# Optimization experiments

Measured on AMD Instinct MI355X. Metric: run time of the kernel, lower is better.

## Reference

```python
import jax, jax.numpy as jnp
import numpy as np
import math

BATCH, D_MODEL, D_STATE, SEQ_L = 8, 256, 64, 2048


def setup_inputs() -> dict:
    key = jax.random.key(0)
    k0, k1, k2, k3 = jax.random.split(key, 4)
    x = jax.random.normal(k0, (BATCH, D_MODEL, SEQ_L), dtype=jnp.float32)
    # A = -exp(A_real) - 1j*A_imag  (S4D-Lin style init: A = -0.5 + i*pi*n)
    A_real = jnp.full((D_MODEL, D_STATE), jnp.log(0.5), dtype=jnp.float32)
    A_imag = -jnp.broadcast_to(math.pi * jnp.arange(D_STATE, dtype=jnp.float32), (D_MODEL, D_STATE))
    # B, C stored as real view of complex: (1, H, N, 2)
    B = jax.random.normal(k1, (1, D_MODEL, D_STATE, 2), dtype=jnp.float32)
    C = jax.random.normal(k2, (1, D_MODEL, D_STATE, 2), dtype=jnp.float32)
    # inv_dt: log-uniform in [log(1e-3), log(1e-1)], shape (H, 1)
    u = jax.random.uniform(k3, (D_MODEL, 1), dtype=jnp.float32)
    inv_dt = u * (math.log(0.1) - math.log(0.001)) + math.log(0.001)
    return {"x": x, "A_real": A_real, "A_imag": A_imag, "B": B, "C": C, "inv_dt": inv_dt}


def reference(x, A_real, A_imag, B, C, inv_dt):
    L = x.shape[-1]
    # --- _get_params ---
    A = -jnp.exp(A_real) - 1j * A_imag            # (H, N) complex poles
    dt = jnp.exp(inv_dt)                           # (H, 1)
    Bc = B[..., 0] + 1j * B[..., 1]                # (1, H, N)
    Cc = C[..., 0] + 1j * C[..., 1]                # (1, H, N)
    # --- compute_kernel ---
    dtA = dt * A                                   # (H, N) = log of discrete-time pole
    Ceff = (Bc * Cc) * (jnp.exp(dtA) - 1.0) / A    # (1, H, N)
    # log-Vandermonde: K = 2*Re sum_n Ceff * exp(dtA)^l  -> (1, H, L)
    ell = jnp.arange(L, dtype=jnp.float32)
    vand = jnp.exp(dtA[:, :, None] * ell)          # (H, N, L) complex
    k = 2.0 * jnp.real(jnp.einsum('chn,hnl->chl', Ceff, vand))  # (1, H, L)
    # --- FFT convolution ---
    n = 2 * L
    k_f = jnp.fft.rfft(k, n=n)                     # (1, H, L+1)
    x_f = jnp.fft.rfft(x, n=n)                     # (B, H, L+1)
    y_f = jnp.einsum('bhl,chl->bchl', x_f, k_f)    # (B, 1, H, L+1)
    y = jnp.fft.irfft(y_f, n=n)[..., :L]           # (B, 1, H, L)
    return jax.nn.relu(y)
```

## Files before the change

kernel.cpp:

```cpp
#include <hip/hip_runtime.h>


#define B_ 8
#define H_ 256
#define N_ 64
#define L_ 2048
#define Q_ 64
#define NC_ 32
#define COLS_ 128
#define PKSTR_ 68
#define PLSTR_ 72

typedef __attribute__((ext_vector_type(8))) short bf16x8;
typedef __attribute__((ext_vector_type(4))) float f32x4;

#define WS_W1R  0
#define WS_W1I  (WS_W1R + 2097152)
#define WS_TL   (WS_W1I + 2097152)
#define WS_W2R  (WS_TL  + 2097152)
#define WS_W2I  (WS_W2R + 2097152)
#define WS_E    (WS_W2I + 2097152)

#if defined(__has_builtin)
#  if __has_builtin(__builtin_amdgcn_cvt_pk_bf16_f32)
#    define HAVE_CVT_PK 1
#  endif
#endif

__device__ __forceinline__ unsigned short bf16_rne(float f) {
    unsigned int u = __float_as_uint(f);
    u += 0x7FFF + ((u >> 16) & 1);
    return (unsigned short)(u >> 16);
}
__device__ __forceinline__ float bf16_to_f(unsigned short h) {
    return __uint_as_float(((unsigned int)h) << 16);
}
__device__ __forceinline__ unsigned int pack_bf16x2(float a, float b) {
#ifdef HAVE_CVT_PK
    typedef __bf16 bf16v2 __attribute__((ext_vector_type(2)));
    bf16v2 p = __builtin_amdgcn_cvt_pk_bf16_f32(a, b);
    return __builtin_bit_cast(unsigned int, p);
#else
    unsigned int ua = __float_as_uint(a);
    ua += 0x7FFF + ((ua >> 16) & 1);
    unsigned int ub = __float_as_uint(b);
    ub += 0x7FFF + ((ub >> 16) & 1);
    return (ua >> 16) | (ub & 0xFFFF0000u);
#endif
}

__global__ __launch_bounds__(256) void s4d_prep(
    const float* __restrict__ A_real, const float* __restrict__ A_imag,
    const float* __restrict__ Bmat, const float* __restrict__ Cmat,
    const float* __restrict__ inv_dt,
    unsigned short* __restrict__ W1sr, unsigned short* __restrict__ W1si,
    unsigned short* __restrict__ TLs,
    unsigned short* __restrict__ W2sr, unsigned short* __restrict__ W2si,
    float2* __restrict__ Earr)
{
    __shared__ float qr_l[65 * 66];
    __shared__ float qi_l[65 * 66];
    __shared__ float klds[64];

    const int h   = blockIdx.x;
    const int tid = threadIdx.x;
    const int n   = tid >> 2;
    const int blk = tid & 3;
    const int hn  = h * N_ + n;

    const float Ar = -expf(A_real[hn]);
    const float Ai = -A_imag[hn];
    const float dtv = expf(inv_dt[h]);
    const float dr = dtv * Ar;
    const float di = dtv * Ai;
    const float ew = expf(dr);
    float sdi, cdi;
    sincosf(di, &sdi, &cdi);
    const float wr = ew * cdi;
    const float wi = ew * sdi;
    const float em1r = wr - 1.0f;
    const float em1i = wi;
    const float invden = 1.0f / (Ar * Ar + Ai * Ai);
    const float tr = (em1r * Ar + em1i * Ai) * invden;
    const float ti = (em1i * Ar - em1r * Ai) * invden;
    const float br = Bmat[2 * hn], bi = Bmat[2 * hn + 1];
    const float cr = Cmat[2 * hn], ci = Cmat[2 * hn + 1];
    const float bcr = br * cr - bi * ci;
    const float bci = br * ci + bi * cr;
    const float Cr = 2.0f * (bcr * tr - bci * ti);
    const float Ci = 2.0f * (bcr * ti + bci * tr);

    {
        const int m0 = 48 - 16 * blk;
        const float e0 = expf((float)m0 * dr);
        float s0, c0;
        sincosf((float)m0 * di, &s0, &c0);
        float pr = e0 * c0, pi = e0 * s0;
        union { unsigned short u16[16]; uint4 q[2]; } tr_, ti_;
        #pragma unroll
        for (int i = 0; i < 16; ++i) {
            tr_.u16[15 - i] = bf16_rne(pr);
            ti_.u16[15 - i] = bf16_rne(pi);
            const float npr = pr * wr - pi * wi;
            pi = pr * wi + pi * wr;
            pr = npr;
        }
        uint4* d0 = (uint4*)(W1sr + (size_t)h * 4096 + n * 64 + blk * 16);
        d0[0] = tr_.q[0]; d0[1] = tr_.q[1];
        uint4* d1 = (uint4*)(W1si + (size_t)h * 4096 + n * 64 + blk * 16);
        d1[0] = ti_.q[0]; d1[1] = ti_.q[1];
    }

    {
        const int m0   = blk * 17;
        const int mcnt = (blk == 3) ? 14 : 17;
        const float e0 = expf((float)m0 * dr);
        float s0, c0;
        sincosf((float)m0 * di, &s0, &c0);
        float pr = e0 * c0, pi = e0 * s0;
        for (int i = 0; i < mcnt; ++i) {
            const int m = m0 + i;
            qr_l[m * 66 + n] = Cr * pr - Ci * pi;
            qi_l[m * 66 + n] = Cr * pi + Ci * pr;
            const float npr = pr * wr - pi * wi;
            pi = pr * wi + pi * wr;
            pr = npr;
        }
    }
    __syncthreads();

    if (tid < 64) {
        float s = 0.0f;
        for (int j = 0; j < 64; ++j) s += qr_l[tid * 66 + j];
        klds[tid] = s;

        const int hn2 = h * N_ + tid;
        const float Ar2 = -expf(A_real[hn2]);
        const float Ai2 = -A_imag[hn2];
        const float e64 = expf(64.0f * dtv * Ar2);
        float s64, c64;
        sincosf(64.0f * dtv * (-Ai2) * -1.0f, &s64, &c64);
        Earr[hn2] = make_float2(e64 * c64, e64 * s64);
    }
    __syncthreads();

    {
        const int t = tid >> 2;
        union { unsigned short u16[16]; uint4 q[2]; } a_, b_;
        #pragma unroll
        for (int i = 0; i < 16; ++i) {
            const int j = blk * 16 + i;
            const int d = t - j;
            a_.u16[i] = bf16_rne(d >= 0 ? klds[d >= 0 ? d : 0] : 0.0f);
        }
        uint4* dtl = (uint4*)(TLs + (size_t)h * 4096 + t * 64 + blk * 16);
        dtl[0] = a_.q[0]; dtl[1] = a_.q[1];

        #pragma unroll
        for (int i = 0; i < 16; ++i) {
            const int nn = blk * 16 + i;
            a_.u16[i] = bf16_rne(qr_l[(t + 1) * 66 + nn]);
            b_.u16[i] = bf16_rne(-qi_l[(t + 1) * 66 + nn]);
        }
        uint4* d2r = (uint4*)(W2sr + (size_t)h * 4096 + t * 64 + blk * 16);
        d2r[0] = a_.q[0]; d2r[1] = a_.q[1];
        uint4* d2i = (uint4*)(W2si + (size_t)h * 4096 + t * 64 + blk * 16);
        d2i[0] = b_.q[0]; d2i[1] = b_.q[1];
    }
}

__global__ __launch_bounds__(256) void s4d_fused(
    const float* __restrict__ x,
    const float2* __restrict__ Earr,
    const unsigned short* __restrict__ W1sr, const unsigned short* __restrict__ W1si,
    const unsigned short* __restrict__ TLs,
    const unsigned short* __restrict__ W2sr, const unsigned short* __restrict__ W2si,
    float* __restrict__ out)
{
    __shared__ char smem[64512];
    unsigned int*   vpk  = (unsigned int*)smem;
    unsigned short* spr  = (unsigned short*)smem;
    unsigned short* spi  = (unsigned short*)(smem + COLS_ * PLSTR_ * 2);
    unsigned short* wreg = (unsigned short*)(smem + COLS_ * PLSTR_ * 4);

    const int h     = blockIdx.x >> 1;
    const int bhalf = blockIdx.x & 1;
    const int tid   = threadIdx.x;
    const int lane  = tid & 63;
    const int wv    = tid >> 6;
    const int colw  = wv * 32;
    const int l15   = lane & 15;
    const int quad  = lane >> 4;

    {
        const unsigned short* s0 = W1sr + (size_t)h * 4096;
        const unsigned short* s1 = W1si + (size_t)h * 4096;
        #pragma unroll
        for (int rep = 0; rep < 2; ++rep) {
            const int idx = rep * 256 + tid;
            const int row = idx >> 3, c8 = (idx & 7) * 8;
            *(uint4*)(wreg + row * PLSTR_ + c8) = *(const uint4*)(s0 + idx * 8);
            *(uint4*)(wreg + 4608 + row * PLSTR_ + c8) = *(const uint4*)(s1 + idx * 8);
        }
    }

    bf16x8 xhi[2][2], xlo[2][2];
    #pragma unroll
    for (int mt = 0; mt < 2; ++mt) {
        const int bc = colw + mt * 16 + l15;
        const int b  = bhalf * 4 + (bc >> 5);
        const int c  = bc & 31;
        const float* xp = x + ((size_t)(b * H_ + h)) * L_ + c * Q_;
        #pragma unroll
        for (int kk = 0; kk < 2; ++kk) {
            const int j0 = kk * 32 + quad * 8;
            const float4 f0 = *(const float4*)(xp + j0);
            const float4 f1 = *(const float4*)(xp + j0 + 4);
            float f[8] = {f0.x, f0.y, f0.z, f0.w, f1.x, f1.y, f1.z, f1.w};
            union { unsigned int u[4]; bf16x8 v; } hi, lo;
            #pragma unroll
            for (int p = 0; p < 4; ++p) {
                const unsigned int hp = pack_bf16x2(f[2 * p], f[2 * p + 1]);
                hi.u[p] = hp;
                const float h0 = __uint_as_float(hp << 16);
                const float h1 = __uint_as_float(hp & 0xFFFF0000u);
                lo.u[p] = pack_bf16x2(f[2 * p] - h0, f[2 * p + 1] - h1);
            }
            xhi[mt][kk] = hi.v;
            xlo[mt][kk] = lo.v;
        }
    }

    const float2 E = Earr[h * N_ + lane];
    const float Er = E.x, Ei = E.y;

    __syncthreads();

    {
        f32x4 accr[2][4], acci[2][4];
        #pragma unroll
        for (int a = 0; a < 2; ++a)
            #pragma unroll
            for (int b = 0; b < 4; ++b) { accr[a][b] = (f32x4)0.0f; acci[a][b] = (f32x4)0.0f; }

        #pragma unroll
        for (int nt = 0; nt < 4; ++nt) {
            const int n = nt * 16 + l15;
            bf16x8 brf[2], bif[2];
            #pragma unroll
            for (int kk = 0; kk < 2; ++kk) {
                const int j0 = kk * 32 + quad * 8;
                brf[kk] = *(const bf16x8*)(wreg + n * PLSTR_ + j0);
                bif[kk] = *(const bf16x8*)(wreg + 4608 + n * PLSTR_ + j0);
            }
            #pragma unroll
            for (int mt = 0; mt < 2; ++mt)
                #pragma unroll
                for (int kk = 0; kk < 2; ++kk) {
                    accr[mt][nt] = __builtin_amdgcn_mfma_f32_16x16x32_bf16(
                        xhi[mt][kk], brf[kk], accr[mt][nt], 0, 0, 0);
                    acci[mt][nt] = __builtin_amdgcn_mfma_f32_16x16x32_bf16(
                        xhi[mt][kk], bif[kk], acci[mt][nt], 0, 0, 0);
                }
        }

        #pragma unroll
        for (int mt = 0; mt < 2; ++mt)
            #pragma unroll
            for (int nt = 0; nt < 4; ++nt)
                #pragma unroll
                for (int r = 0; r < 4; ++r) {
                    const int bc = colw + mt * 16 + quad * 4 + r;
                    const int n  = nt * 16 + l15;
                    vpk[bc * PKSTR_ + n] =
                        pack_bf16x2(accr[mt][nt][r], acci[mt][nt][r]);
                }
    }
    __syncthreads();

    {
        unsigned int vv[NC_];
        const unsigned int* vp = &vpk[(wv * NC_) * PKSTR_ + lane];
        #pragma unroll
        for (int c = 0; c < NC_; ++c) vv[c] = vp[c * PKSTR_];

        {
            const unsigned short* s0 = TLs  + (size_t)h * 4096;
            const unsigned short* s1 = W2sr + (size_t)h * 4096;
            const unsigned short* s2 = W2si + (size_t)h * 4096;
            #pragma unroll
            for (int rep = 0; rep < 2; ++rep) {
                const int idx = rep * 256 + tid;
                const int row = idx >> 3, c8 = (idx & 7) * 8;
                *(uint4*)(wreg + row * PLSTR_ + c8) = *(const uint4*)(s0 + idx * 8);
                *(uint4*)(wreg + 4608 + row * PLSTR_ + c8) = *(const uint4*)(s1 + idx * 8);
                *(uint4*)(wreg + 9216 + row * PLSTR_ + c8) = *(const uint4*)(s2 + idx * 8);
            }
        }
        __syncthreads();

        float sr = 0.0f, si = 0.0f;
        unsigned short* pr = &spr[(wv * NC_) * PLSTR_ + lane];
        unsigned short* pi = &spi[(wv * NC_) * PLSTR_ + lane];
        #pragma unroll
        for (int c = 0; c < NC_; ++c) {
            const float vr = __uint_as_float(vv[c] << 16);
            const float vi = __uint_as_float(vv[c] & 0xFFFF0000u);
            const unsigned int sp2 = pack_bf16x2(sr, si);
            pr[c * PLSTR_] = (unsigned short)(sp2 & 0xFFFFu);
            pi[c * PLSTR_] = (unsigned short)(sp2 >> 16);
            const float nsr = fmaf(Er, sr, fmaf(-Ei, si, vr));
            si = fmaf(Ei, sr, fmaf(Er, si, vi));
            sr = nsr;
        }
    }
    __syncthreads();

    {
        bf16x8 sr8[2][2], si8[2][2];
        #pragma unroll
        for (int mt = 0; mt < 2; ++mt) {
            const int bc = colw + mt * 16 + l15;
            #pragma unroll
            for (int kk = 0; kk < 2; ++kk) {
                const int j0 = kk * 32 + quad * 8;
                sr8[mt][kk] = *(const bf16x8*)(&spr[bc * PLSTR_ + j0]);
                si8[mt][kk] = *(const bf16x8*)(&spi[bc * PLSTR_ + j0]);
            }
        }

        f32x4 acc[2][4];
        #pragma unroll
        for (int a = 0; a < 2; ++a)
            #pragma unroll
            for (int t = 0; t < 4; ++t) acc[a][t] = (f32x4)0.0f;

        #pragma unroll
        for (int tt = 0; tt < 4; ++tt) {
            const int t = tt * 16 + l15;
            bf16x8 btl[2], bwr[2], bwi[2];
            #pragma unroll
            for (int kk = 0; kk < 2; ++kk) {
                const int j0 = kk * 32 + quad * 8;
                btl[kk] = *(const bf16x8*)(wreg + t * PLSTR_ + j0);
                bwr[kk] = *(const bf16x8*)(wreg + 4608 + t * PLSTR_ + j0);
                bwi[kk] = *(const bf16x8*)(wreg + 9216 + t * PLSTR_ + j0);
            }
            #pragma unroll
            for (int mt = 0; mt < 2; ++mt)
                #pragma unroll
                for (int kk = 0; kk < 2; ++kk) {
                    acc[mt][tt] = __builtin_amdgcn_mfma_f32_16x16x32_bf16(
                        xhi[mt][kk], btl[kk], acc[mt][tt], 0, 0, 0);
                    acc[mt][tt] = __builtin_amdgcn_mfma_f32_16x16x32_bf16(
                        xlo[mt][kk], btl[kk], acc[mt][tt], 0, 0, 0);
                    acc[mt][tt] = __builtin_amdgcn_mfma_f32_16x16x32_bf16(
                        sr8[mt][kk], bwr[kk], acc[mt][tt], 0, 0, 0);
                    acc[mt][tt] = __builtin_amdgcn_mfma_f32_16x16x32_bf16(
                        si8[mt][kk], bwi[kk], acc[mt][tt], 0, 0, 0);
                }
        }

        #pragma unroll
        for (int mt = 0; mt < 2; ++mt)
            #pragma unroll
            for (int tt = 0; tt < 4; ++tt)
                #pragma unroll
                for (int r = 0; r < 4; ++r) {
                    const int bc = colw + mt * 16 + quad * 4 + r;
                    const int b  = bhalf * 4 + (bc >> 5);
                    const int c  = bc & 31;
                    const int t  = tt * 16 + l15;
                    out[((size_t)(b * H_ + h)) * L_ + c * Q_ + t] =
                        fmaxf(acc[mt][tt][r], 0.0f);
                }
    }
}

extern "C" void kernel_launch(void* const* d_in, const int* in_sizes, int n_in,
                              void* d_out, int out_size, void* d_ws, size_t ws_size,
                              hipStream_t stream) {
    const float* x      = (const float*)d_in[0];
    const float* A_real = (const float*)d_in[1];
    const float* A_imag = (const float*)d_in[2];
    const float* Bmat   = (const float*)d_in[3];
    const float* Cmat   = (const float*)d_in[4];
    const float* inv_dt = (const float*)d_in[5];
    float* out = (float*)d_out;

    char* ws = (char*)d_ws;
    unsigned short* W1sr = (unsigned short*)(ws + WS_W1R);
    unsigned short* W1si = (unsigned short*)(ws + WS_W1I);
    unsigned short* TLs  = (unsigned short*)(ws + WS_TL);
    unsigned short* W2sr = (unsigned short*)(ws + WS_W2R);
    unsigned short* W2si = (unsigned short*)(ws + WS_W2I);
    float2*         Earr = (float2*)(ws + WS_E);

    s4d_prep<<<dim3(H_), dim3(256), 0, stream>>>(
        A_real, A_imag, Bmat, Cmat, inv_dt, W1sr, W1si, TLs, W2sr, W2si, Earr);
    s4d_fused<<<dim3(H_ * 2), dim3(256), 0, stream>>>(
        x, Earr, W1sr, W1si, TLs, W2sr, W2si, out);
}
```

Measured before the change: 90.21 us.

## Fuse parameter prep kernel into main kernel, building weights directly in LDS

```diff
diff --git a/kernel.cpp b/kernel.cpp
--- a/kernel.cpp
+++ b/kernel.cpp
@@ -14,13 +14,6 @@
 typedef __attribute__((ext_vector_type(8))) short bf16x8;
 typedef __attribute__((ext_vector_type(4))) float f32x4;
 
-#define WS_W1R  0
-#define WS_W1I  (WS_W1R + 2097152)
-#define WS_TL   (WS_W1I + 2097152)
-#define WS_W2R  (WS_TL  + 2097152)
-#define WS_W2I  (WS_W2R + 2097152)
-#define WS_E    (WS_W2I + 2097152)
-
 #if defined(__has_builtin)
 #  if __has_builtin(__builtin_amdgcn_cvt_pk_bf16_f32)
 #    define HAVE_CVT_PK 1
@@ -31,9 +24,6 @@
     unsigned int u = __float_as_uint(f);
     u += 0x7FFF + ((u >> 16) & 1);
     return (unsigned short)(u >> 16);
-}
-__device__ __forceinline__ float bf16_to_f(unsigned short h) {
-    return __uint_as_float(((unsigned int)h) << 16);
 }
 __device__ __forceinline__ unsigned int pack_bf16x2(float a, float b) {
 #ifdef HAVE_CVT_PK
@@ -49,139 +39,24 @@
 #endif
 }
 
-__global__ __launch_bounds__(256) void s4d_prep(
+__global__ __launch_bounds__(256, 2) void s4d_one(
+    const float* __restrict__ x,
     const float* __restrict__ A_real, const float* __restrict__ A_imag,
     const float* __restrict__ Bmat, const float* __restrict__ Cmat,
     const float* __restrict__ inv_dt,
-    unsigned short* __restrict__ W1sr, unsigned short* __restrict__ W1si,
-    unsigned short* __restrict__ TLs,
-    unsigned short* __restrict__ W2sr, unsigned short* __restrict__ W2si,
-    float2* __restrict__ Earr)
-{
-    __shared__ float qr_l[65 * 66];
-    __shared__ float qi_l[65 * 66];
-    __shared__ float klds[64];
-
-    const int h   = blockIdx.x;
-    const int tid = threadIdx.x;
-    const int n   = tid >> 2;
-    const int blk = tid & 3;
-    const int hn  = h * N_ + n;
-
-    const float Ar = -expf(A_real[hn]);
-    const float Ai = -A_imag[hn];
-    const float dtv = expf(inv_dt[h]);
-    const float dr = dtv * Ar;
-    const float di = dtv * Ai;
-    const float ew = expf(dr);
-    float sdi, cdi;
-    sincosf(di, &sdi, &cdi);
-    const float wr = ew * cdi;
-    const float wi = ew * sdi;
-    const float em1r = wr - 1.0f;
-    const float em1i = wi;
-    const float invden = 1.0f / (Ar * Ar + Ai * Ai);
-    const float tr = (em1r * Ar + em1i * Ai) * invden;
-    const float ti = (em1i * Ar - em1r * Ai) * invden;
-    const float br = Bmat[2 * hn], bi = Bmat[2 * hn + 1];
-    const float cr = Cmat[2 * hn], ci = Cmat[2 * hn + 1];
-    const float bcr = br * cr - bi * ci;
-    const float bci = br * ci + bi * cr;
-    const float Cr = 2.0f * (bcr * tr - bci * ti);
-    const float Ci = 2.0f * (bcr * ti + bci * tr);
-
-    {
-        const int m0 = 48 - 16 * blk;
-        const float e0 = expf((float)m0 * dr);
-        float s0, c0;
-        sincosf((float)m0 * di, &s0, &c0);
-        float pr = e0 * c0, pi = e0 * s0;
-        union { unsigned short u16[16]; uint4 q[2]; } tr_, ti_;
-        #pragma unroll
-        for (int i = 0; i < 16; ++i) {
-            tr_.u16[15 - i] = bf16_rne(pr);
-            ti_.u16[15 - i] = bf16_rne(pi);
-            const float npr = pr * wr - pi * wi;
-            pi = pr * wi + pi * wr;
-            pr = npr;
-        }
-        uint4* d0 = (uint4*)(W1sr + (size_t)h * 4096 + n * 64 + blk * 16);
-        d0[0] = tr_.q[0]; d0[1] = tr_.q[1];
-        uint4* d1 = (uint4*)(W1si + (size_t)h * 4096 + n * 64 + blk * 16);
-        d1[0] = ti_.q[0]; d1[1] = ti_.q[1];
-    }
-
-    {
-        const int m0   = blk * 17;
-        const int mcnt = (blk == 3) ? 14 : 17;
-        const float e0 = expf((float)m0 * dr);
-        float s0, c0;
-        sincosf((float)m0 * di, &s0, &c0);
-        float pr = e0 * c0, pi = e0 * s0;
-        for (int i = 0; i < mcnt; ++i) {
-            const int m = m0 + i;
-            qr_l[m * 66 + n] = Cr * pr - Ci * pi;
-            qi_l[m * 66 + n] = Cr * pi + Ci * pr;
-            const float npr = pr * wr - pi * wi;
-            pi = pr * wi + pi * wr;
-            pr = npr;
-        }
-    }
-    __syncthreads();
-
-    if (tid < 64) {
-        float s = 0.0f;
-        for (int j = 0; j < 64; ++j) s += qr_l[tid * 66 + j];
-        klds[tid] = s;
-
-        const int hn2 = h * N_ + tid;
-        const float Ar2 = -expf(A_real[hn2]);
-        const float Ai2 = -A_imag[hn2];
-        const float e64 = expf(64.0f * dtv * Ar2);
-        float s64, c64;
-        sincosf(64.0f * dtv * (-Ai2) * -1.0f, &s64, &c64);
-        Earr[hn2] = make_float2(e64 * c64, e64 * s64);
-    }
-    __syncthreads();
-
-    {
-        const int t = tid >> 2;
-        union { unsigned short u16[16]; uint4 q[2]; } a_, b_;
-        #pragma unroll
-        for (int i = 0; i < 16; ++i) {
-            const int j = blk * 16 + i;
-            const int d = t - j;
-            a_.u16[i] = bf16_rne(d >= 0 ? klds[d >= 0 ? d : 0] : 0.0f);
-        }
-        uint4* dtl = (uint4*)(TLs + (size_t)h * 4096 + t * 64 + blk * 16);
-        dtl[0] = a_.q[0]; dtl[1] = a_.q[1];
-
-        #pragma unroll
-        for (int i = 0; i < 16; ++i) {
-            const int nn = blk * 16 + i;
-            a_.u16[i] = bf16_rne(qr_l[(t + 1) * 66 + nn]);
-            b_.u16[i] = bf16_rne(-qi_l[(t + 1) * 66 + nn]);
-        }
-        uint4* d2r = (uint4*)(W2sr + (size_t)h * 4096 + t * 64 + blk * 16);
-        d2r[0] = a_.q[0]; d2r[1] = a_.q[1];
-        uint4* d2i = (uint4*)(W2si + (size_t)h * 4096 + t * 64 + blk * 16);
-        d2i[0] = b_.q[0]; d2i[1] = b_.q[1];
-    }
-}
-
-__global__ __launch_bounds__(256) void s4d_fused(
-    const float* __restrict__ x,
-    const float2* __restrict__ Earr,
-    const unsigned short* __restrict__ W1sr, const unsigned short* __restrict__ W1si,
-    const unsigned short* __restrict__ TLs,
-    const unsigned short* __restrict__ W2sr, const unsigned short* __restrict__ W2si,
     float* __restrict__ out)
 {
-    __shared__ char smem[64512];
+    __shared__ __align__(16) char smem[81664];
+    float*          qr_l = (float*)smem;
+    float*          qi_l = (float*)(smem + 17160);
     unsigned int*   vpk  = (unsigned int*)smem;
     unsigned short* spr  = (unsigned short*)smem;
-    unsigned short* spi  = (unsigned short*)(smem + COLS_ * PLSTR_ * 2);
-    unsigned short* wreg = (unsigned short*)(smem + COLS_ * PLSTR_ * 4);
+    unsigned short* spi  = (unsigned short*)(smem + 18432);
+    unsigned short* w1r  = (unsigned short*)(smem + 34816);
+    unsigned short* w1i  = (unsigned short*)(smem + 44032);
+    unsigned short* wreg = (unsigned short*)(smem + 53248);
+    float2*         eLDS = (float2*)(smem + 80896);
+    float*          klds = (float*)(smem + 81408);
 
     const int h     = blockIdx.x >> 1;
     const int bhalf = blockIdx.x & 1;
@@ -192,19 +67,7 @@
     const int l15   = lane & 15;
     const int quad  = lane >> 4;
 
-    {
-        const unsigned short* s0 = W1sr + (size_t)h * 4096;
-        const unsigned short* s1 = W1si + (size_t)h * 4096;
-        #pragma unroll
-        for (int rep = 0; rep < 2; ++rep) {
-            const int idx = rep * 256 + tid;
-            const int row = idx >> 3, c8 = (idx & 7) * 8;
-            *(uint4*)(wreg + row * PLSTR_ + c8) = *(const uint4*)(s0 + idx * 8);
-            *(uint4*)(wreg + 4608 + row * PLSTR_ + c8) = *(const uint4*)(s1 + idx * 8);
-        }
-    }
-
-    bf16x8 xhi[2][2], xlo[2][2];
+    float4 xraw[2][2][2];
     #pragma unroll
     for (int mt = 0; mt < 2; ++mt) {
         const int bc = colw + mt * 16 + l15;
@@ -214,8 +77,128 @@
         #pragma unroll
         for (int kk = 0; kk < 2; ++kk) {
             const int j0 = kk * 32 + quad * 8;
-            const float4 f0 = *(const float4*)(xp + j0);
-            const float4 f1 = *(const float4*)(xp + j0 + 4);
+            xraw[mt][kk][0] = *(const float4*)(xp + j0);
+            xraw[mt][kk][1] = *(const float4*)(xp + j0 + 4);
+        }
+    }
+
+    const int n   = tid >> 2;
+    const int blk = tid & 3;
+    const int hn  = h * N_ + n;
+    {
+        const float Ar = -expf(A_real[hn]);
+        const float Ai = -A_imag[hn];
+        const float dtv = expf(inv_dt[h]);
+        const float dr = dtv * Ar;
+        const float di = dtv * Ai;
+        const float ew = expf(dr);
+        float sdi, cdi;
+        sincosf(di, &sdi, &cdi);
+        const float wr = ew * cdi;
+        const float wi = ew * sdi;
+        const float em1r = wr - 1.0f;
+        const float em1i = wi;
+        const float invden = 1.0f / (Ar * Ar + Ai * Ai);
+        const float tr = (em1r * Ar + em1i * Ai) * invden;
+        const float ti = (em1i * Ar - em1r * Ai) * invden;
+        const float br = Bmat[2 * hn], bi = Bmat[2 * hn + 1];
+        const float cr = Cmat[2 * hn], ci = Cmat[2 * hn + 1];
+        const float bcr = br * cr - bi * ci;
+        const float bci = br * ci + bi * cr;
+        const float Cr = 2.0f * (bcr * tr - bci * ti);
+        const float Ci = 2.0f * (bcr * ti + bci * tr);
+
+        {
+            const int m0 = 48 - 16 * blk;
+            const float e0 = expf((float)m0 * dr);
+            float s0, c0;
+            sincosf((float)m0 * di, &s0, &c0);
+            float pr = e0 * c0, pi = e0 * s0;
+            union { unsigned short u16[16]; uint4 q[2]; } tr_, ti_;
+            #pragma unroll
+            for (int i = 0; i < 16; ++i) {
+                tr_.u16[15 - i] = bf16_rne(pr);
+                ti_.u16[15 - i] = bf16_rne(pi);
+                const float npr = pr * wr - pi * wi;
+                pi = pr * wi + pi * wr;
+                pr = npr;
+            }
+            uint4* d0 = (uint4*)(w1r + n * PLSTR_ + blk * 16);
+            d0[0] = tr_.q[0]; d0[1] = tr_.q[1];
+            uint4* d1 = (uint4*)(w1i + n * PLSTR_ + blk * 16);
+            d1[0] = ti_.q[0]; d1[1] = ti_.q[1];
+        }
+        {
+            const int m0   = blk * 17;
+            const int mcnt = (blk == 3) ? 14 : 17;
+            const float e0 = expf((float)m0 * dr);
+            float s0, c0;
+            sincosf((float)m0 * di, &s0, &c0);
+            float pr = e0 * c0, pi = e0 * s0;
+            for (int i = 0; i < mcnt; ++i) {
+                const int m = m0 + i;
+                qr_l[m * 66 + n] = Cr * pr - Ci * pi;
+                qi_l[m * 66 + n] = Cr * pi + Ci * pr;
+                const float npr = pr * wr - pi * wi;
+                pi = pr * wi + pi * wr;
+                pr = npr;
+            }
+        }
+    }
+    __syncthreads();
+
+    {
+        const int t = tid >> 2;
+        float s = 0.0f;
+        #pragma unroll
+        for (int i = 0; i < 16; ++i) s += qr_l[t * 66 + blk * 16 + i];
+        s += __shfl_xor(s, 1);
+        s += __shfl_xor(s, 2);
+        if (blk == 0) klds[t] = s;
+    }
+    if (tid < 64) {
+        const int hn2 = h * N_ + tid;
+        const float Ar2 = -expf(A_real[hn2]);
+        const float Ai2 = -A_imag[hn2];
+        const float dtv = expf(inv_dt[h]);
+        const float e64 = expf(64.0f * dtv * Ar2);
+        float s64, c64;
+        sincosf(64.0f * dtv * Ai2, &s64, &c64);
+        eLDS[tid] = make_float2(e64 * c64, e64 * s64);
+    }
+    __syncthreads();
+
+    {
+        const int t = tid >> 2;
+        union { unsigned short u16[16]; uint4 q[2]; } a_, b_;
+        #pragma unroll
+        for (int i = 0; i < 16; ++i) {
+            const int j = blk * 16 + i;
+            const int d = t - j;
+            a_.u16[i] = bf16_rne(d >= 0 ? klds[d >= 0 ? d : 0] : 0.0f);
+        }
+        uint4* dtl = (uint4*)(wreg + t * PLSTR_ + blk * 16);
+        dtl[0] = a_.q[0]; dtl[1] = a_.q[1];
+
+        #pragma unroll
+        for (int i = 0; i < 16; ++i) {
+            const int nn = blk * 16 + i;
+            a_.u16[i] = bf16_rne(qr_l[(t + 1) * 66 + nn]);
+            b_.u16[i] = bf16_rne(-qi_l[(t + 1) * 66 + nn]);
+        }
+        uint4* d2r = (uint4*)(wreg + 4608 + t * PLSTR_ + blk * 16);
+        d2r[0] = a_.q[0]; d2r[1] = a_.q[1];
+        uint4* d2i = (uint4*)(wreg + 9216 + t * PLSTR_ + blk * 16);
+        d2i[0] = b_.q[0]; d2i[1] = b_.q[1];
+    }
+
+    bf16x8 xhi[2][2], xlo[2][2];
+    #pragma unroll
+    for (int mt = 0; mt < 2; ++mt)
+        #pragma unroll
+        for (int kk = 0; kk < 2; ++kk) {
+            const float4 f0 = xraw[mt][kk][0];
+            const float4 f1 = xraw[mt][kk][1];
             float f[8] = {f0.x, f0.y, f0.z, f0.w, f1.x, f1.y, f1.z, f1.w};
             union { unsigned int u[4]; bf16x8 v; } hi, lo;
             #pragma unroll
@@ -229,9 +212,8 @@
             xhi[mt][kk] = hi.v;
             xlo[mt][kk] = lo.v;
         }
-    }
-
-    const float2 E = Earr[h * N_ + lane];
+
+    const float2 E = eLDS[lane];
     const float Er = E.x, Ei = E.y;
 
     __syncthreads();
@@ -245,13 +227,13 @@
 
         #pragma unroll
         for (int nt = 0; nt < 4; ++nt) {
-            const int n = nt * 16 + l15;
+            const int nn = nt * 16 + l15;
             bf16x8 brf[2], bif[2];
             #pragma unroll
             for (int kk = 0; kk < 2; ++kk) {
                 const int j0 = kk * 32 + quad * 8;
-                brf[kk] = *(const bf16x8*)(wreg + n * PLSTR_ + j0);
-                bif[kk] = *(const bf16x8*)(wreg + 4608 + n * PLSTR_ + j0);
+                brf[kk] = *(const bf16x8*)(w1r + nn * PLSTR_ + j0);
+                bif[kk] = *(const bf16x8*)(w1i + nn * PLSTR_ + j0);
             }
             #pragma unroll
             for (int mt = 0; mt < 2; ++mt)
@@ -271,8 +253,8 @@
                 #pragma unroll
                 for (int r = 0; r < 4; ++r) {
                     const int bc = colw + mt * 16 + quad * 4 + r;
-                    const int n  = nt * 16 + l15;
-                    vpk[bc * PKSTR_ + n] =
+                    const int nn = nt * 16 + l15;
+                    vpk[bc * PKSTR_ + nn] =
                         pack_bf16x2(accr[mt][nt][r], acci[mt][nt][r]);
                 }
     }
@@ -283,20 +265,6 @@
         const unsigned int* vp = &vpk[(wv * NC_) * PKSTR_ + lane];
         #pragma unroll
         for (int c = 0; c < NC_; ++c) vv[c] = vp[c * PKSTR_];
-
-        {
-            const unsigned short* s0 = TLs  + (size_t)h * 4096;
-            const unsigned short* s1 = W2sr + (size_t)h * 4096;
-            const unsigned short* s2 = W2si + (size_t)h * 4096;
-            #pragma unroll
-            for (int rep = 0; rep < 2; ++rep) {
-                const int idx = rep * 256 + tid;
-                const int row = idx >> 3, c8 = (idx & 7) * 8;
-                *(uint4*)(wreg + row * PLSTR_ + c8) = *(const uint4*)(s0 + idx * 8);
-                *(uint4*)(wreg + 4608 + row * PLSTR_ + c8) = *(const uint4*)(s1 + idx * 8);
-                *(uint4*)(wreg + 9216 + row * PLSTR_ + c8) = *(const uint4*)(s2 + idx * 8);
-            }
-        }
         __syncthreads();
 
         float sr = 0.0f, si = 0.0f;
@@ -387,17 +355,8 @@
     const float* Cmat   = (const float*)d_in[4];
     const float* inv_dt = (const float*)d_in[5];
     float* out = (float*)d_out;
-
-    char* ws = (char*)d_ws;
-    unsigned short* W1sr = (unsigned short*)(ws + WS_W1R);
-    unsigned short* W1si = (unsigned short*)(ws + WS_W1I);
-    unsigned short* TLs  = (unsigned short*)(ws + WS_TL);
-    unsigned short* W2sr = (unsigned short*)(ws + WS_W2R);
-    unsigned short* W2si = (unsigned short*)(ws + WS_W2I);
-    float2*         Earr = (float2*)(ws + WS_E);
-
-    s4d_prep<<<dim3(H_), dim3(256), 0, stream>>>(
-        A_real, A_imag, Bmat, Cmat, inv_dt, W1sr, W1si, TLs, W2sr, W2si, Earr);
-    s4d_fused<<<dim3(H_ * 2), dim3(256), 0, stream>>>(
-        x, Earr, W1sr, W1si, TLs, W2sr, W2si, out);
+    (void)d_ws; (void)ws_size;
+
+    s4d_one<<<dim3(H_ * 2), dim3(256), 0, stream>>>(
+        x, A_real, A_imag, Bmat, Cmat, inv_dt, out);
 }
```

Result: faster. 87.90 us (-2.6%).
